# Performance work log

Hardware: AMD Instinct MI355X
Metric: run time of the kernel (lower is better)

Reference implementation:

```python
import jax, jax.numpy as jnp
import numpy as np

ALPHA = 0.2  # LeakyReLU negative slope
NEG_FILL = -9e15


def setup_inputs() -> dict:
    key = jax.random.key(0)
    k_adj, k_x, k_W, k_a = jax.random.split(key, 4)
    n, in_feats, out_feats = 12288, 256, 64
    adj = jax.random.randint(k_adj, (n, n), 0, 2, dtype=jnp.int32)
    x = jax.random.normal(k_x, (n, in_feats), dtype=jnp.float32)
    W = jax.random.normal(k_W, (in_feats, out_feats), dtype=jnp.float32) * 0.1
    a = jax.random.normal(k_a, (2 * out_feats, 1), dtype=jnp.float32) * 0.1
    return {"adj": adj, "x": x, "W": W, "a": a}


def reference(adj, x, W, a):
    out_feats = W.shape[1]
    h = x @ W                                  # (n, out_feats)
    wh1 = h @ a[:out_feats]                    # (n, 1)
    wh2 = h @ a[out_feats:]                    # (n, 1)
    e = jax.nn.leaky_relu(wh1 + wh2, ALPHA)    # (n, 1) -- faithful to source (no transpose)
    # broadcast (n,1) scores against (n,n) adjacency mask
    attention = jnp.where(adj > 0, e, NEG_FILL)
    attention = jax.nn.softmax(attention, axis=1)
    # dropout p=0.0 -> identity (eval mode)
    h_prime = attention @ h                    # (n, out_feats)
    return jax.nn.elu(h_prime)                 # concat=True
```

## Files before the change

kernel.cpp:

```cpp
#include <hip/hip_runtime.h>

#define N_NODES 12288
#define IN_F    256
#define OUT_F   64
#define KSPLIT  8
#define MT      64
#define KC      (N_NODES / KSPLIT)
#define BK      128
#define NSTEP   (KC / BK)
#define NSTRH   (N_NODES + 32)
#define LPAD    8

typedef __attribute__((ext_vector_type(8))) short bf16x8;
typedef __attribute__((ext_vector_type(4))) float f32x4;

__device__ __forceinline__ unsigned short f2bf(float f) {
    union { float f; unsigned int i; } v; v.f = f;
    unsigned int x = v.i;
    unsigned int r = x + 0x7FFFu + ((x >> 16) & 1u);
    return (unsigned short)(r >> 16);
}

__global__ __launch_bounds__(256) void k_hT(const float* __restrict__ x,
                                            const float* __restrict__ W,
                                            unsigned short* __restrict__ hT) {
    __shared__ unsigned short WT[OUT_F][IN_F + 8];
    int tid = threadIdx.x;
    for (int idx = tid; idx < IN_F * OUT_F; idx += 256) {
        int k = idx >> 6, n = idx & 63;
        WT[n][k] = f2bf(W[idx]);
    }
    __syncthreads();

    int lane = tid & 63, wave = tid >> 6;
    int q = lane >> 4, ml = lane & 15;
    int i0 = blockIdx.x * MT;
    int row = i0 + 16 * wave + ml;
    const float* xr = x + (size_t)row * IN_F + 8 * q;

    f32x4 acc[4];
    #pragma unroll
    for (int nt = 0; nt < 4; ++nt) acc[nt] = (f32x4){0.f, 0.f, 0.f, 0.f};

    #pragma unroll
    for (int kk = 0; kk < IN_F; kk += 32) {
        float4 x0 = *(const float4*)(xr + kk);
        float4 x1 = *(const float4*)(xr + kk + 4);
        union { bf16x8 v; unsigned short u[8]; } A;
        A.u[0] = f2bf(x0.x); A.u[1] = f2bf(x0.y); A.u[2] = f2bf(x0.z); A.u[3] = f2bf(x0.w);
        A.u[4] = f2bf(x1.x); A.u[5] = f2bf(x1.y); A.u[6] = f2bf(x1.z); A.u[7] = f2bf(x1.w);
        #pragma unroll
        for (int nt = 0; nt < 4; ++nt) {
            bf16x8 bv = *(const bf16x8*)&WT[16 * nt + ml][kk + 8 * q];
            acc[nt] = __builtin_amdgcn_mfma_f32_16x16x32_bf16(A.v, bv, acc[nt], 0, 0, 0);
        }
    }

    #pragma unroll
    for (int nt = 0; nt < 4; ++nt) {
        ushort4 o;
        o.x = f2bf(acc[nt][0]); o.y = f2bf(acc[nt][1]);
        o.z = f2bf(acc[nt][2]); o.w = f2bf(acc[nt][3]);
        *(ushort4*)&hT[(size_t)(16 * nt + ml) * NSTRH + i0 + 16 * wave + 4 * q] = o;
    }
}

__global__ __launch_bounds__(256) void k_spmm(const int* __restrict__ adj,
                                              const unsigned short* __restrict__ hT,
                                              float* __restrict__ s_part,
                                              float* __restrict__ deg_part) {
    __shared__ unsigned short As[MT][BK + LPAD];
    __shared__ unsigned short Bs[OUT_F][BK + LPAD];

    const int tid  = threadIdx.x;
    const int lane = tid & 63;
    const int wave = tid >> 6;
    const int q    = lane >> 4;
    const int ml   = lane & 15;
    const int i0   = blockIdx.x * MT;
    const int ks   = blockIdx.y;
    const int k0   = ks * KC;

    const int ar  = tid >> 5;
    const int ac4 = tid & 31;
    const int* ap = adj + (size_t)(i0 + ar) * N_NODES + k0 + 4 * ac4;

    const int br  = tid >> 4;
    const int bc8 = (tid & 15) * 8;
    const unsigned short* bp = hT + (size_t)br * NSTRH + k0 + bc8;

    union { bf16x8 v; unsigned short u[8]; } ones;
    #pragma unroll
    for (int i = 0; i < 8; ++i) ones.u[i] = 0x3F80;

    f32x4 acc[4], accd;
    #pragma unroll
    for (int nt = 0; nt < 4; ++nt) acc[nt] = (f32x4){0.f, 0.f, 0.f, 0.f};
    accd = (f32x4){0.f, 0.f, 0.f, 0.f};

    int4  a[8];
    uint4 b[4];

#define LOADT(s) do {                                                          \
    _Pragma("unroll")                                                          \
    for (int j = 0; j < 8; ++j)                                                \
        a[j] = *(const int4*)(ap + (size_t)8 * j * N_NODES + (s) * BK);        \
    _Pragma("unroll")                                                          \
    for (int j = 0; j < 4; ++j)                                                \
        b[j] = *(const uint4*)(bp + (size_t)16 * j * NSTRH + (s) * BK);        \
} while (0)

#define WRITET() do {                                                          \
    _Pragma("unroll")                                                          \
    for (int j = 0; j < 8; ++j) {                                              \
        unsigned int lo = ((unsigned int)a[j].x + ((unsigned int)a[j].y << 16)) * 0x3F80u; \
        unsigned int hi = ((unsigned int)a[j].z + ((unsigned int)a[j].w << 16)) * 0x3F80u; \
        unsigned int* d = (unsigned int*)&As[ar + 8 * j][4 * ac4];             \
        d[0] = lo; d[1] = hi;                                                  \
    }                                                                          \
    _Pragma("unroll")                                                          \
    for (int j = 0; j < 4; ++j)                                                \
        *(uint4*)&Bs[br + 16 * j][bc8] = b[j];                                 \
} while (0)

    LOADT(0);

    for (int s = 0; s < NSTEP; ++s) {
        WRITET();
        __syncthreads();

        if (s + 1 < NSTEP) LOADT(s + 1);

        #pragma unroll
        for (int kk = 0; kk < BK; kk += 32) {
            bf16x8 av = *(const bf16x8*)&As[16 * wave + ml][kk + 8 * q];
            #pragma unroll
            for (int nt = 0; nt < 4; ++nt) {
                bf16x8 bv = *(const bf16x8*)&Bs[16 * nt + ml][kk + 8 * q];
                acc[nt] = __builtin_amdgcn_mfma_f32_16x16x32_bf16(av, bv, acc[nt], 0, 0, 0);
            }
            accd = __builtin_amdgcn_mfma_f32_16x16x32_bf16(av, ones.v, accd, 0, 0, 0);
        }

        __syncthreads();
    }

#undef LOADT
#undef WRITET

    float* sp = s_part + (size_t)ks * ((size_t)N_NODES * OUT_F);
    #pragma unroll
    for (int nt = 0; nt < 4; ++nt) {
        #pragma unroll
        for (int rr = 0; rr < 4; ++rr) {
            int orow = i0 + 16 * wave + 4 * q + rr;
            int ocol = 16 * nt + ml;
            sp[(size_t)orow * OUT_F + ocol] = acc[nt][rr];
        }
    }

    if (ml == 0) {
        #pragma unroll
        for (int rr = 0; rr < 4; ++rr)
            deg_part[ks * N_NODES + i0 + 16 * wave + 4 * q + rr] = accd[rr];
    }
}

__global__ __launch_bounds__(256) void k_out(const float* __restrict__ s_part,
                                             const float* __restrict__ deg_part,
                                             float* __restrict__ out) {
    int idx = blockIdx.x * 256 + threadIdx.x;
    int i = idx >> 6;
    float s = 0.f, deg = 0.f;
    #pragma unroll
    for (int p = 0; p < KSPLIT; ++p) {
        s   += s_part[(size_t)p * ((size_t)N_NODES * OUT_F) + idx];
        deg += deg_part[p * N_NODES + i];
    }
    float v = (deg > 0.5f) ? (s / deg) : 0.f;
    out[idx] = (v > 0.f) ? v : expm1f(v);
}

extern "C" void kernel_launch(void* const* d_in, const int* in_sizes, int n_in,
                              void* d_out, int out_size, void* d_ws, size_t ws_size,
                              hipStream_t stream) {
    const int*   adj = (const int*)d_in[0];
    const float* x   = (const float*)d_in[1];
    const float* W   = (const float*)d_in[2];
    float* out = (float*)d_out;

    char* ws = (char*)d_ws;
    const size_t hT_bytes  = (size_t)OUT_F * NSTRH * 2;
    const size_t sp_bytes  = (size_t)KSPLIT * N_NODES * OUT_F * 4;
    unsigned short* hT     = (unsigned short*)ws;
    float* s_part          = (float*)(ws + hT_bytes);
    float* deg_part        = (float*)(ws + hT_bytes + sp_bytes);

    k_hT  <<<dim3(N_NODES / MT),          dim3(256), 0, stream>>>(x, W, hT);
    k_spmm<<<dim3(N_NODES / MT, KSPLIT),  dim3(256), 0, stream>>>(adj, hT, s_part, deg_part);
    k_out <<<dim3(N_NODES * OUT_F / 256), dim3(256), 0, stream>>>(s_part, deg_part, out);
}
```

Baseline: 833.7 us.

## Bit-pack adjacency in a separate pass and stage whole K-chunks in LDS

Adds a k_bitpack kernel that turns the int32 adjacency matrix into a bitmask using wave ballots. The SpMM then reads compact bits instead of int32 tiles, and KSPLIT rises to 32 so each block loads its whole hT chunk and bit slice into shared memory once, with no double-buffered loop. The int32 adjacency is still read once, by the bitpack pass, and the kernel unpacks bits to bf16 in registers. The cost is a fourfold larger partial-sum buffer for k_out to reduce and one extra launch.

```diff
diff --git a/kernel.cpp b/kernel.cpp
--- a/kernel.cpp
+++ b/kernel.cpp
@@ -3,13 +3,11 @@
 #define N_NODES 12288
 #define IN_F    256
 #define OUT_F   64
-#define KSPLIT  8
+#define KSPLIT  32
 #define MT      64
 #define KC      (N_NODES / KSPLIT)
-#define BK      128
-#define NSTEP   (KC / BK)
 #define NSTRH   (N_NODES + 32)
-#define LPAD    8
+#define ABSTR   1600
 
 typedef __attribute__((ext_vector_type(8))) short bf16x8;
 typedef __attribute__((ext_vector_type(4))) float f32x4;
@@ -19,6 +17,32 @@
     unsigned int x = v.i;
     unsigned int r = x + 0x7FFFu + ((x >> 16) & 1u);
     return (unsigned short)(r >> 16);
+}
+
+__global__ __launch_bounds__(256) void k_bitpack(const int* __restrict__ adj,
+                                                 unsigned char* __restrict__ abits) {
+    const int tid  = threadIdx.x;
+    const int lane = tid & 63;
+    const int wave = tid >> 6;
+    const int row  = blockIdx.x * 2 + (wave >> 1);
+    const int half = wave & 1;
+
+    const int* src = adj + (size_t)row * N_NODES + half * (N_NODES / 2) + lane;
+    unsigned long long* dst =
+        (unsigned long long*)(abits + (size_t)row * ABSTR + half * (N_NODES / 16));
+
+    const int iters = (N_NODES / 2) / 64;
+    int a0 = src[0];
+    int a1 = src[64];
+    for (int i = 0; i < iters - 2; ++i) {
+        int a2 = src[(size_t)(i + 2) * 64];
+        unsigned long long m = __ballot(a0 != 0);
+        if (lane == 0) dst[i] = m;
+        a0 = a1; a1 = a2;
+    }
+    unsigned long long m0 = __ballot(a0 != 0);
+    unsigned long long m1 = __ballot(a1 != 0);
+    if (lane == 0) { dst[iters - 2] = m0; dst[iters - 1] = m1; }
 }
 
 __global__ __launch_bounds__(256) void k_hT(const float* __restrict__ x,
@@ -65,12 +89,12 @@
     }
 }
 
-__global__ __launch_bounds__(256) void k_spmm(const int* __restrict__ adj,
+__global__ __launch_bounds__(256) void k_spmm(const unsigned char* __restrict__ abits,
                                               const unsigned short* __restrict__ hT,
                                               float* __restrict__ s_part,
                                               float* __restrict__ deg_part) {
-    __shared__ unsigned short As[MT][BK + LPAD];
-    __shared__ unsigned short Bs[OUT_F][BK + LPAD];
+    __shared__ unsigned short Bs[OUT_F][KC + 8];
+    __shared__ unsigned char  Ab[MT][52];
 
     const int tid  = threadIdx.x;
     const int lane = tid & 63;
@@ -81,13 +105,26 @@
     const int ks   = blockIdx.y;
     const int k0   = ks * KC;
 
-    const int ar  = tid >> 5;
-    const int ac4 = tid & 31;
-    const int* ap = adj + (size_t)(i0 + ar) * N_NODES + k0 + 4 * ac4;
-
-    const int br  = tid >> 4;
-    const int bc8 = (tid & 15) * 8;
-    const unsigned short* bp = hT + (size_t)br * NSTRH + k0 + bc8;
+    {
+        const int brow = 16 * wave + (lane >> 2);
+        const int bco  = (lane & 3) * 8;
+        const unsigned short* bp = hT + (size_t)brow * NSTRH + k0 + bco;
+        #pragma unroll
+        for (int j = 0; j < 12; ++j) {
+            uint4 v = *(const uint4*)(bp + 32 * j);
+            *(uint4*)&Bs[brow][bco + 32 * j] = v;
+        }
+    }
+    {
+        const int arow = tid >> 2;
+        const int apart = (tid & 3) * 12;
+        const unsigned int* asrc =
+            (const unsigned int*)(abits + (size_t)(i0 + arow) * ABSTR + ks * (KC / 8) + apart);
+        unsigned int d0 = asrc[0], d1 = asrc[1], d2 = asrc[2];
+        unsigned int* ad = (unsigned int*)&Ab[arow][apart];
+        ad[0] = d0; ad[1] = d1; ad[2] = d2;
+    }
+    __syncthreads();
 
     union { bf16x8 v; unsigned short u[8]; } ones;
     #pragma unroll
@@ -98,55 +135,23 @@
     for (int nt = 0; nt < 4; ++nt) acc[nt] = (f32x4){0.f, 0.f, 0.f, 0.f};
     accd = (f32x4){0.f, 0.f, 0.f, 0.f};
 
-    int4  a[8];
-    uint4 b[4];
-
-#define LOADT(s) do {                                                          \
-    _Pragma("unroll")                                                          \
-    for (int j = 0; j < 8; ++j)                                                \
-        a[j] = *(const int4*)(ap + (size_t)8 * j * N_NODES + (s) * BK);        \
-    _Pragma("unroll")                                                          \
-    for (int j = 0; j < 4; ++j)                                                \
-        b[j] = *(const uint4*)(bp + (size_t)16 * j * NSTRH + (s) * BK);        \
-} while (0)
-
-#define WRITET() do {                                                          \
-    _Pragma("unroll")                                                          \
-    for (int j = 0; j < 8; ++j) {                                              \
-        unsigned int lo = ((unsigned int)a[j].x + ((unsigned int)a[j].y << 16)) * 0x3F80u; \
-        unsigned int hi = ((unsigned int)a[j].z + ((unsigned int)a[j].w << 16)) * 0x3F80u; \
-        unsigned int* d = (unsigned int*)&As[ar + 8 * j][4 * ac4];             \
-        d[0] = lo; d[1] = hi;                                                  \
-    }                                                                          \
-    _Pragma("unroll")                                                          \
-    for (int j = 0; j < 4; ++j)                                                \
-        *(uint4*)&Bs[br + 16 * j][bc8] = b[j];                                 \
-} while (0)
-
-    LOADT(0);
-
-    for (int s = 0; s < NSTEP; ++s) {
-        WRITET();
-        __syncthreads();
-
-        if (s + 1 < NSTEP) LOADT(s + 1);
-
-        #pragma unroll
-        for (int kk = 0; kk < BK; kk += 32) {
-            bf16x8 av = *(const bf16x8*)&As[16 * wave + ml][kk + 8 * q];
-            #pragma unroll
-            for (int nt = 0; nt < 4; ++nt) {
-                bf16x8 bv = *(const bf16x8*)&Bs[16 * nt + ml][kk + 8 * q];
-                acc[nt] = __builtin_amdgcn_mfma_f32_16x16x32_bf16(av, bv, acc[nt], 0, 0, 0);
-            }
-            accd = __builtin_amdgcn_mfma_f32_16x16x32_bf16(av, ones.v, accd, 0, 0, 0);
-        }
-
-        __syncthreads();
-    }
-
-#undef LOADT
-#undef WRITET
+    const int arow = 16 * wave + ml;
+    #pragma unroll
+    for (int kk = 0; kk < KC; kk += 32) {
+        unsigned int b = Ab[arow][(kk >> 3) + q];
+        union { bf16x8 v; unsigned int w[4]; } av;
+        av.w[0] = (b & 1u) * 0x3F80u         + (b & 2u) * 0x1FC00000u;
+        av.w[1] = ((b >> 2) & 1u) * 0x3F80u  + ((b >> 2) & 2u) * 0x1FC00000u;
+        av.w[2] = ((b >> 4) & 1u) * 0x3F80u  + ((b >> 4) & 2u) * 0x1FC00000u;
+        av.w[3] = ((b >> 6) & 1u) * 0x3F80u  + ((b >> 6) & 2u) * 0x1FC00000u;
+
+        #pragma unroll
+        for (int nt = 0; nt < 4; ++nt) {
+            bf16x8 bv = *(const bf16x8*)&Bs[16 * nt + ml][kk + 8 * q];
+            acc[nt] = __builtin_amdgcn_mfma_f32_16x16x32_bf16(av.v, bv, acc[nt], 0, 0, 0);
+        }
+        accd = __builtin_amdgcn_mfma_f32_16x16x32_bf16(av.v, ones.v, accd, 0, 0, 0);
+    }
 
     float* sp = s_part + (size_t)ks * ((size_t)N_NODES * OUT_F);
     #pragma unroll
@@ -190,13 +195,16 @@
     float* out = (float*)d_out;
 
     char* ws = (char*)d_ws;
-    const size_t hT_bytes  = (size_t)OUT_F * NSTRH * 2;
-    const size_t sp_bytes  = (size_t)KSPLIT * N_NODES * OUT_F * 4;
-    unsigned short* hT     = (unsigned short*)ws;
-    float* s_part          = (float*)(ws + hT_bytes);
-    float* deg_part        = (float*)(ws + hT_bytes + sp_bytes);
-
-    k_hT  <<<dim3(N_NODES / MT),          dim3(256), 0, stream>>>(x, W, hT);
-    k_spmm<<<dim3(N_NODES / MT, KSPLIT),  dim3(256), 0, stream>>>(adj, hT, s_part, deg_part);
-    k_out <<<dim3(N_NODES * OUT_F / 256), dim3(256), 0, stream>>>(s_part, deg_part, out);
-}
+    const size_t hT_bytes = (size_t)OUT_F * NSTRH * 2;
+    const size_t sp_bytes = (size_t)KSPLIT * N_NODES * OUT_F * 4;
+    const size_t dp_bytes = (size_t)KSPLIT * N_NODES * 4;
+    unsigned short* hT   = (unsigned short*)ws;
+    float* s_part        = (float*)(ws + hT_bytes);
+    float* deg_part      = (float*)(ws + hT_bytes + sp_bytes);
+    unsigned char* abits = (unsigned char*)(ws + hT_bytes + sp_bytes + dp_bytes);
+
+    k_bitpack<<<dim3(N_NODES / 2),          dim3(256), 0, stream>>>(adj, abits);
+    k_hT     <<<dim3(N_NODES / MT),         dim3(256), 0, stream>>>(x, W, hT);
+    k_spmm   <<<dim3(N_NODES / MT, KSPLIT), dim3(256), 0, stream>>>(abits, hT, s_part, deg_part);
+    k_out    <<<dim3(N_NODES * OUT_F / 256),dim3(256), 0, stream>>>(s_part, deg_part, out);
+}
```

New measurement: 878.9 us. +5.4%, slower.
